# Performance work log

Measured on AMD Instinct MI355X. Metric: run time of the kernel, lower is better.

## Reference

```python
import jax, jax.numpy as jnp
import numpy as np

BN_EPS = 1e-5
HEADS = 8

def _bn(y, gamma, beta, mean, var):
    # eval-mode BatchNorm2d over channel axis 1; y: [B,C,H,W]
    scale = gamma / jnp.sqrt(var + BN_EPS)
    shift = beta - mean * scale
    return y * scale[None, :, None, None] + shift[None, :, None, None]

def setup_inputs() -> dict:
    key = jax.random.key(0)
    ks = jax.random.split(key, 12)
    B, C, H, W = 16, 256, 64, 64
    x = jax.random.normal(ks[0], (B, C, H, W), jnp.float32)
    qkv_w = jax.random.normal(ks[1], (3 * C, C), jnp.float32) * 0.05
    qkv_gamma = jax.random.uniform(ks[2], (3 * C,), jnp.float32, 0.5, 1.5)
    qkv_beta = jax.random.normal(ks[3], (3 * C,), jnp.float32) * 0.1
    qkv_mean = jax.random.normal(ks[4], (3 * C,), jnp.float32) * 0.1
    qkv_var = jax.random.uniform(ks[5], (3 * C,), jnp.float32, 0.5, 1.5)
    proj_w = jax.random.normal(ks[6], (C, C), jnp.float32) * 0.05
    proj_gamma = jax.random.uniform(ks[7], (C,), jnp.float32, 0.5, 1.5)
    proj_beta = jax.random.normal(ks[8], (C,), jnp.float32) * 0.1
    proj_mean = jax.random.normal(ks[9], (C,), jnp.float32) * 0.1
    proj_var = jax.random.uniform(ks[10], (C,), jnp.float32, 0.5, 1.5)
    return {"x": x, "qkv_w": qkv_w, "qkv_gamma": qkv_gamma, "qkv_beta": qkv_beta,
            "qkv_mean": qkv_mean, "qkv_var": qkv_var, "proj_w": proj_w,
            "proj_gamma": proj_gamma, "proj_beta": proj_beta,
            "proj_mean": proj_mean, "proj_var": proj_var}

def reference(x, qkv_w, qkv_gamma, qkv_beta, qkv_mean, qkv_var,
              proj_w, proj_gamma, proj_beta, proj_mean, proj_var):
    B, C, H, W = x.shape
    hd = C // HEADS  # head_dim
    # 1x1 conv (no bias) + BN
    qkv = jnp.einsum('bchw,oc->bohw', x, qkv_w)
    qkv = _bn(qkv, qkv_gamma, qkv_beta, qkv_mean, qkv_var)
    q, k, v = jnp.split(qkv, 3, axis=1)
    N = H * W
    q = q.reshape(B, HEADS, hd, N)
    k = k.reshape(B, HEADS, hd, N)
    v = v.reshape(B, HEADS, hd, N)
    q = jax.nn.softmax(q, axis=-1)   # over tokens
    k = jax.nn.softmax(k, axis=-2)   # over head_dim
    context = jnp.einsum('bhdn,bhen->bhde', k, v)   # [B,h,d,d]
    out = jnp.einsum('bhdn,bhde->bhen', q, context) # [B,h,d,N]
    out = out.reshape(B, C, H, W)
    out = jnp.einsum('bchw,oc->bohw', out, proj_w)
    out = _bn(out, proj_gamma, proj_beta, proj_mean, proj_var)
    return out
```

## Files before the change

kernel.cpp:

```cpp
#include <hip/hip_runtime.h>

typedef unsigned short ushort_t;
typedef unsigned int u32;
typedef short short8 __attribute__((ext_vector_type(8)));
typedef short short4_t __attribute__((ext_vector_type(4)));
typedef float f32x4 __attribute__((ext_vector_type(4)));
typedef float f32x16 __attribute__((ext_vector_type(16)));

#define NTOK 4096
#define NCOLS 65536
#define CIN 256

__device__ __forceinline__ float b2f(ushort_t u) {
    union { unsigned int i; float f; } v; v.i = ((unsigned int)u) << 16; return v.f;
}
__device__ __forceinline__ ushort_t f2b(float f) {
    union { float f; unsigned int i; } v; v.f = f;
    unsigned int r = v.i + 0x7FFFu + ((v.i >> 16) & 1u);
    return (ushort_t)(r >> 16);
}

__device__ __forceinline__ void gl_lds16(const ushort_t* g, ushort_t* l) {
    __builtin_amdgcn_global_load_lds(
        (const __attribute__((address_space(1))) u32*)(const void*)g,
        (__attribute__((address_space(3))) u32*)(void*)l,
        16, 0, 0);
}

__global__ __launch_bounds__(256) void cvt_w(const float* __restrict__ wq,
                                             const float* __restrict__ wp,
                                             ushort_t* __restrict__ wqb,
                                             ushort_t* __restrict__ wpb,
                                             float* __restrict__ scz) {
    int i = blockIdx.x * 256 + threadIdx.x;
    if (i < 768 * 256) wqb[i] = f2b(wq[i]);
    else               wpb[i - 768 * 256] = f2b(wp[i - 768 * 256]);
    if (i < 131072) scz[i] = 0.f;
}

__global__ __launch_bounds__(256) void transpose_x(const float* __restrict__ x,
                                                   ushort_t* __restrict__ xt) {
    __shared__ ushort_t lds[64 * 264];
    int tid = threadIdx.x;
    int g0 = blockIdx.x * 64;
    int b = g0 >> 12, n0 = g0 & 4095;
    const float* src = x + (size_t)b * (CIN * NTOK);
    int tn = tid & 63, cg = tid >> 6;
    for (int c4 = 0; c4 < 64; c4++) {
        int c = c4 * 4 + cg;
        lds[tn * 264 + c] = f2b(src[(size_t)c * NTOK + n0 + tn]);
    }
    __syncthreads();
    int tok = tid >> 2, c8 = (tid & 3) * 8;
    ushort_t* dst = xt + (size_t)(g0 + tok) * CIN + c8;
#pragma unroll
    for (int j = 0; j < 8; j++)
        *(short8*)(dst + j * 32) = *(const short8*)&lds[tok * 264 + c8 + j * 32];
}

__global__ __launch_bounds__(256) void gemm128(const ushort_t* __restrict__ W,
                                               const ushort_t* __restrict__ Xc,
                                               const float* __restrict__ gamma,
                                               const float* __restrict__ beta,
                                               const float* __restrict__ mean,
                                               const float* __restrict__ var,
                                               ushort_t* __restrict__ out_b,
                                               float* __restrict__ out_f, int mode) {
    __shared__ __align__(16) ushort_t lA[2][128 * 32];
    __shared__ __align__(16) ushort_t lB[2][128 * 32];
    int tid = threadIdx.x;
    int wave = tid >> 6, lane = tid & 63;
    int l15 = lane & 15, q = lane >> 4;
    int mh = wave >> 1, nh = wave & 1;
    int m0 = blockIdx.x * 128, colb = blockIdx.y * 128;

    f32x4 acc[4][4];
#pragma unroll
    for (int i = 0; i < 4; i++)
#pragma unroll
        for (int j = 0; j < 4; j++)
#pragma unroll
            for (int r = 0; r < 4; r++) acc[i][j][r] = 0.f;

    const ushort_t* gA0 = W  + (size_t)(m0 +      (tid >> 2)) * CIN + (tid & 3) * 8;
    const ushort_t* gA1 = W  + (size_t)(m0 + 64 + (tid >> 2)) * CIN + (tid & 3) * 8;
    const ushort_t* gB0 = Xc + (size_t)(colb +      (tid >> 2)) * CIN + (tid & 3) * 8;
    const ushort_t* gB1 = Xc + (size_t)(colb + 64 + (tid >> 2)) * CIN + (tid & 3) * 8;
    int so0 = tid * 8;
    int so1 = 2048 + tid * 8;

    gl_lds16(gA0,      &lA[0][so0]);
    gl_lds16(gA1,      &lA[0][so1]);
    gl_lds16(gB0,      &lB[0][so0]);
    gl_lds16(gB1,      &lB[0][so1]);
    gl_lds16(gA0 + 32, &lA[1][so0]);
    gl_lds16(gA1 + 32, &lA[1][so1]);
    gl_lds16(gB0 + 32, &lB[1][so0]);
    gl_lds16(gB1 + 32, &lB[1][so1]);

#pragma unroll
    for (int t = 0; t < 8; t++) {
        const int cur = t & 1;
        if (t < 7) asm volatile("s_waitcnt vmcnt(4)" ::: "memory");
        else       asm volatile("s_waitcnt vmcnt(0)" ::: "memory");
        __builtin_amdgcn_s_barrier();

        short8 af[4], bf[4];
#pragma unroll
        for (int i = 0; i < 4; i++) {
            af[i] = *(const short8*)&lA[cur][(mh * 64 + i * 16 + l15) * 32 + q * 8];
            bf[i] = *(const short8*)&lB[cur][(nh * 64 + i * 16 + l15) * 32 + q * 8];
        }
#pragma unroll
        for (int mi = 0; mi < 4; mi++)
#pragma unroll
            for (int ni = 0; ni < 4; ni++)
                acc[mi][ni] = __builtin_amdgcn_mfma_f32_16x16x32_bf16(af[mi], bf[ni],
                                                                      acc[mi][ni], 0, 0, 0);
        __builtin_amdgcn_s_barrier();
        if (t < 6) {
            int k0 = (t + 2) * 32;
            gl_lds16(gA0 + k0, &lA[cur][so0]);
            gl_lds16(gA1 + k0, &lA[cur][so1]);
            gl_lds16(gB0 + k0, &lB[cur][so0]);
            gl_lds16(gB1 + k0, &lB[cur][so1]);
        }
    }

    int col_l = colb + nh * 64 + l15;
#pragma unroll
    for (int mi = 0; mi < 4; mi++) {
#pragma unroll
        for (int r = 0; r < 4; r++) {
            int m = m0 + mh * 64 + mi * 16 + q * 4 + r;
            float sc = gamma[m] * rsqrtf(var[m] + 1e-5f);
            float sh = beta[m] - mean[m] * sc;
#pragma unroll
            for (int ni = 0; ni < 4; ni++) {
                float val = acc[mi][ni][r] * sc + sh;
                int col = col_l + ni * 16;
                if (mode == 0) {
                    out_b[(size_t)m * NCOLS + col] = f2b(val);
                } else {
                    int bb = col >> 12, n = col & 4095;
                    out_f[(size_t)bb * (CIN * NTOK) + (size_t)m * NTOK + n] = val;
                }
            }
        }
    }
}

__global__ __launch_bounds__(256) void qsum_ker(const ushort_t* __restrict__ qkv,
                                                float* __restrict__ qsums) {
    int tid = threadIdx.x, wave = tid >> 6, lane = tid & 63;
    int rid = blockIdx.x * 4 + wave;
    int c = rid >> 4, b = rid & 15;
    const ushort_t* row = qkv + (size_t)c * NCOLS + b * NTOK;
    float s = 0.f;
#pragma unroll
    for (int j = 0; j < 8; j++) {
        short8 pk = *(const short8*)(row + j * 512 + lane * 8);
#pragma unroll
        for (int i = 0; i < 8; i++) s += __expf(b2f((ushort_t)pk[i]));
    }
    for (int off = 1; off < 64; off <<= 1) s += __shfl_xor(s, off);
    if (lane == 0) qsums[c * 16 + b] = s;
}

__global__ __launch_bounds__(256) void ctx_ker(const ushort_t* __restrict__ qkv,
                                               float* __restrict__ ctxbuf) {
    int sl = blockIdx.x, bh = blockIdx.y;
    int b = bh >> 3, h = bh & 7;
    int tid = threadIdx.x, wave = tid >> 6, lane = tid & 63;
    int l31 = lane & 31, l5 = lane >> 5;
    int col0 = b * NTOK + sl * 512 + wave * 128;
    const ushort_t* krow = qkv + (size_t)(256 + h * 32 + l31) * NCOLS + col0 + l5 * 8;
    const ushort_t* vrow = qkv + (size_t)(512 + h * 32 + l31) * NCOLS + col0 + l5 * 8;
    f32x16 acc;
#pragma unroll
    for (int i = 0; i < 16; i++) acc[i] = 0.f;
#pragma unroll
    for (int st = 0; st < 8; st++) {
        short8 kf = *(const short8*)(krow + st * 16);
        short8 vf = *(const short8*)(vrow + st * 16);
        short8 af;
#pragma unroll
        for (int j = 0; j < 8; j++) {
            float e = __expf(b2f((ushort_t)kf[j]));
            float t = e;
            t += __shfl_xor(t, 1);
            t += __shfl_xor(t, 2);
            t += __shfl_xor(t, 4);
            t += __shfl_xor(t, 8);
            t += __shfl_xor(t, 16);
            af[j] = (short)f2b(__fdividef(e, t));
        }
        acc = __builtin_amdgcn_mfma_f32_32x32x16_bf16(af, vf, acc, 0, 0, 0);
    }
    __shared__ float red[4][1024];
#pragma unroll
    for (int r = 0; r < 16; r++) {
        int d = (r & 3) + 8 * (r >> 2) + 4 * l5;
        red[wave][d * 32 + l31] = acc[r];
    }
    __syncthreads();
    int i0 = tid * 4;
#pragma unroll
    for (int i = 0; i < 4; i++) {
        int idx = i0 + i;
        float v = red[0][idx] + red[1][idx] + red[2][idx] + red[3][idx];
        atomicAdd(ctxbuf + (size_t)bh * 1024 + idx, v);
    }
}

__global__ __launch_bounds__(256) void out_ker(const ushort_t* __restrict__ qkv,
                                               const float* __restrict__ ctxbuf,
                                               const float* __restrict__ qsums,
                                               ushort_t* __restrict__ attT) {
    int sl = blockIdx.x, bh = blockIdx.y;
    int b = bh >> 3, h = bh & 7;
    int tid = threadIdx.x, wave = tid >> 6, lane = tid & 63;
    int l31 = lane & 31, l5 = lane >> 5;
    __shared__ __align__(16) ushort_t ctxT[32 * 40];
    __shared__ __align__(16) ushort_t qT[256 * 40];
    __shared__ __align__(16) ushort_t obuf[4][32 * 40];

#pragma unroll
    for (int i = 0; i < 4; i++) {
        int idx = tid * 4 + i;
        int d = idx >> 5, e = idx & 31;
        ctxT[e * 40 + d] = f2b(ctxbuf[(size_t)bh * 1024 + idx]);
    }
    __syncthreads();
    short8 a0 = *(const short8*)(ctxT + l31 * 40 + l5 * 8);
    short8 a1 = *(const short8*)(ctxT + l31 * 40 + 16 + l5 * 8);

    const ushort_t* qbase = qkv + (size_t)(h * 32) * NCOLS;
    int segbase = b * NTOK + sl * 512;
    int d = tid & 31, t8 = (tid >> 5) * 8;
    float sq = 1.f / qsums[(h * 32 + d) * 16 + b];

    for (int nc = 0; nc < 2; nc++) {
        int gcol0 = segbase + nc * 256;
#pragma unroll
        for (int jj = 0; jj < 4; jj++) {
            int tok8 = jj * 64 + t8;
            short8 pk = *(const short8*)(qbase + (size_t)d * NCOLS + gcol0 + tok8);
#pragma unroll
            for (int j = 0; j < 8; j++)
                qT[(tok8 + j) * 40 + d] = f2b(__expf(b2f((ushort_t)pk[j])) * sq);
        }
        __syncthreads();
#pragma unroll
        for (int ti = 0; ti < 2; ti++) {
            int tok0 = (wave + ti * 4) * 32;
            f32x16 acc;
#pragma unroll
            for (int i = 0; i < 16; i++) acc[i] = 0.f;
            short8 b0 = *(const short8*)(qT + (size_t)(tok0 + l31) * 40 + l5 * 8);
            short8 b1 = *(const short8*)(qT + (size_t)(tok0 + l31) * 40 + 16 + l5 * 8);
            acc = __builtin_amdgcn_mfma_f32_32x32x16_bf16(a0, b0, acc, 0, 0, 0);
            acc = __builtin_amdgcn_mfma_f32_32x32x16_bf16(a1, b1, acc, 0, 0, 0);
#pragma unroll
            for (int r = 0; r < 16; r++) {
                int e = (r & 3) + 8 * (r >> 2) + 4 * l5;
                obuf[wave][l31 * 40 + e] = f2b(acc[r]);
            }
            __syncthreads();
            {
                int tok = lane >> 1, half = lane & 1;
                const ushort_t* srcp = &obuf[wave][tok * 40 + half * 16];
                short8 r0 = *(const short8*)srcp;
                short8 r1 = *(const short8*)(srcp + 8);
                size_t g = (size_t)(gcol0 + tok0 + tok) * 256 + h * 32 + half * 16;
                *(short8*)(attT + g) = r0;
                *(short8*)(attT + g + 8) = r1;
            }
            __syncthreads();
        }
        __syncthreads();
    }
}

extern "C" void kernel_launch(void* const* d_in, const int* in_sizes, int n_in,
                              void* d_out, int out_size, void* d_ws, size_t ws_size,
                              hipStream_t stream) {
    const float* x          = (const float*)d_in[0];
    const float* qkv_w      = (const float*)d_in[1];
    const float* qkv_gamma  = (const float*)d_in[2];
    const float* qkv_beta   = (const float*)d_in[3];
    const float* qkv_mean   = (const float*)d_in[4];
    const float* qkv_var    = (const float*)d_in[5];
    const float* proj_w     = (const float*)d_in[6];
    const float* proj_gamma = (const float*)d_in[7];
    const float* proj_beta  = (const float*)d_in[8];
    const float* proj_mean  = (const float*)d_in[9];
    const float* proj_var   = (const float*)d_in[10];

    ushort_t* wqb = (ushort_t*)d_ws;
    ushort_t* wpb = wqb + 768 * 256;
    ushort_t* xt  = wpb + 256 * 256;
    ushort_t* qkv = xt + (size_t)NCOLS * CIN;
    float* out    = (float*)d_out;
    float* ctxbuf = (float*)d_out;
    float* qsums  = ctxbuf + 131072;

    cvt_w<<<1024, 256, 0, stream>>>(qkv_w, proj_w, wqb, wpb, ctxbuf);
    transpose_x<<<1024, 256, 0, stream>>>(x, xt);
    gemm128<<<dim3(6, 512), 256, 0, stream>>>(wqb, xt, qkv_gamma, qkv_beta,
                                              qkv_mean, qkv_var, qkv, nullptr, 0);
    qsum_ker<<<1024, 256, 0, stream>>>(qkv, qsums);
    ctx_ker<<<dim3(8, 128), 256, 0, stream>>>(qkv, ctxbuf);
    out_ker<<<dim3(8, 128), 256, 0, stream>>>(qkv, ctxbuf, qsums, xt);
    gemm128<<<dim3(2, 512), 256, 0, stream>>>(wpb, xt, proj_gamma, proj_beta,
                                              proj_mean, proj_var, nullptr, out, 1);
}
```

Baseline: 299.6 us.

## Enlarge GEMM tile to 256x128 with 512 threads and reorder grid

```diff
diff --git a/kernel.cpp b/kernel.cpp
--- a/kernel.cpp
+++ b/kernel.cpp
@@ -58,7 +58,7 @@
         *(short8*)(dst + j * 32) = *(const short8*)&lds[tok * 264 + c8 + j * 32];
 }
 
-__global__ __launch_bounds__(256) void gemm128(const ushort_t* __restrict__ W,
+__global__ __launch_bounds__(512) void gemm256(const ushort_t* __restrict__ W,
                                                const ushort_t* __restrict__ Xc,
                                                const float* __restrict__ gamma,
                                                const float* __restrict__ beta,
@@ -66,13 +66,13 @@
                                                const float* __restrict__ var,
                                                ushort_t* __restrict__ out_b,
                                                float* __restrict__ out_f, int mode) {
-    __shared__ __align__(16) ushort_t lA[2][128 * 32];
+    __shared__ __align__(16) ushort_t lA[2][256 * 32];
     __shared__ __align__(16) ushort_t lB[2][128 * 32];
     int tid = threadIdx.x;
     int wave = tid >> 6, lane = tid & 63;
     int l15 = lane & 15, q = lane >> 4;
-    int mh = wave >> 1, nh = wave & 1;
-    int m0 = blockIdx.x * 128, colb = blockIdx.y * 128;
+    int mq = wave >> 1, nq = wave & 1;
+    int m0 = blockIdx.y * 256, colb = blockIdx.x * 128;
 
     f32x4 acc[4][4];
 #pragma unroll
@@ -82,34 +82,32 @@
 #pragma unroll
             for (int r = 0; r < 4; r++) acc[i][j][r] = 0.f;
 
-    const ushort_t* gA0 = W  + (size_t)(m0 +      (tid >> 2)) * CIN + (tid & 3) * 8;
-    const ushort_t* gA1 = W  + (size_t)(m0 + 64 + (tid >> 2)) * CIN + (tid & 3) * 8;
-    const ushort_t* gB0 = Xc + (size_t)(colb +      (tid >> 2)) * CIN + (tid & 3) * 8;
-    const ushort_t* gB1 = Xc + (size_t)(colb + 64 + (tid >> 2)) * CIN + (tid & 3) * 8;
-    int so0 = tid * 8;
-    int so1 = 2048 + tid * 8;
-
-    gl_lds16(gA0,      &lA[0][so0]);
-    gl_lds16(gA1,      &lA[0][so1]);
-    gl_lds16(gB0,      &lB[0][so0]);
-    gl_lds16(gB1,      &lB[0][so1]);
-    gl_lds16(gA0 + 32, &lA[1][so0]);
-    gl_lds16(gA1 + 32, &lA[1][so1]);
-    gl_lds16(gB0 + 32, &lB[1][so0]);
-    gl_lds16(gB1 + 32, &lB[1][so1]);
+    const ushort_t* gA0 = W  + (size_t)(m0 +       (tid >> 2)) * CIN + (tid & 3) * 8;
+    const ushort_t* gA1 = W  + (size_t)(m0 + 128 + (tid >> 2)) * CIN + (tid & 3) * 8;
+    const ushort_t* gB0 = Xc + (size_t)(colb +     (tid >> 2)) * CIN + (tid & 3) * 8;
+    int sa0 = tid * 8;
+    int sa1 = 4096 + tid * 8;
+    int sb0 = tid * 8;
+
+    gl_lds16(gA0,      &lA[0][sa0]);
+    gl_lds16(gA1,      &lA[0][sa1]);
+    gl_lds16(gB0,      &lB[0][sb0]);
+    gl_lds16(gA0 + 32, &lA[1][sa0]);
+    gl_lds16(gA1 + 32, &lA[1][sa1]);
+    gl_lds16(gB0 + 32, &lB[1][sb0]);
 
 #pragma unroll
     for (int t = 0; t < 8; t++) {
         const int cur = t & 1;
-        if (t < 7) asm volatile("s_waitcnt vmcnt(4)" ::: "memory");
+        if (t < 7) asm volatile("s_waitcnt vmcnt(3)" ::: "memory");
         else       asm volatile("s_waitcnt vmcnt(0)" ::: "memory");
         __builtin_amdgcn_s_barrier();
 
         short8 af[4], bf[4];
 #pragma unroll
         for (int i = 0; i < 4; i++) {
-            af[i] = *(const short8*)&lA[cur][(mh * 64 + i * 16 + l15) * 32 + q * 8];
-            bf[i] = *(const short8*)&lB[cur][(nh * 64 + i * 16 + l15) * 32 + q * 8];
+            af[i] = *(const short8*)&lA[cur][(mq * 64 + i * 16 + l15) * 32 + q * 8];
+            bf[i] = *(const short8*)&lB[cur][(nq * 64 + i * 16 + l15) * 32 + q * 8];
         }
 #pragma unroll
         for (int mi = 0; mi < 4; mi++)
@@ -120,19 +118,18 @@
         __builtin_amdgcn_s_barrier();
         if (t < 6) {
             int k0 = (t + 2) * 32;
-            gl_lds16(gA0 + k0, &lA[cur][so0]);
-            gl_lds16(gA1 + k0, &lA[cur][so1]);
-            gl_lds16(gB0 + k0, &lB[cur][so0]);
-            gl_lds16(gB1 + k0, &lB[cur][so1]);
-        }
-    }
-
-    int col_l = colb + nh * 64 + l15;
+            gl_lds16(gA0 + k0, &lA[cur][sa0]);
+            gl_lds16(gA1 + k0, &lA[cur][sa1]);
+            gl_lds16(gB0 + k0, &lB[cur][sb0]);
+        }
+    }
+
+    int col_l = colb + nq * 64 + l15;
 #pragma unroll
     for (int mi = 0; mi < 4; mi++) {
 #pragma unroll
         for (int r = 0; r < 4; r++) {
-            int m = m0 + mh * 64 + mi * 16 + q * 4 + r;
+            int m = m0 + mq * 64 + mi * 16 + q * 4 + r;
             float sc = gamma[m] * rsqrtf(var[m] + 1e-5f);
             float sh = beta[m] - mean[m] * sc;
 #pragma unroll
@@ -307,11 +304,11 @@
 
     cvt_w<<<1024, 256, 0, stream>>>(qkv_w, proj_w, wqb, wpb, ctxbuf);
     transpose_x<<<1024, 256, 0, stream>>>(x, xt);
-    gemm128<<<dim3(6, 512), 256, 0, stream>>>(wqb, xt, qkv_gamma, qkv_beta,
+    gemm256<<<dim3(512, 3), 512, 0, stream>>>(wqb, xt, qkv_gamma, qkv_beta,
                                               qkv_mean, qkv_var, qkv, nullptr, 0);
     qsum_ker<<<1024, 256, 0, stream>>>(qkv, qsums);
     ctx_ker<<<dim3(8, 128), 256, 0, stream>>>(qkv, ctxbuf);
     out_ker<<<dim3(8, 128), 256, 0, stream>>>(qkv, ctxbuf, qsums, xt);
-    gemm128<<<dim3(2, 512), 256, 0, stream>>>(wpb, xt, proj_gamma, proj_beta,
+    gemm256<<<dim3(512, 1), 512, 0, stream>>>(wpb, xt, proj_gamma, proj_beta,
                                               proj_mean, proj_var, nullptr, out, 1);
 }
```

Result: no change. 303.8 us (+1.4%).
